# Performance work log

Measured on AMD Instinct MI355X. Metric: run time of the kernel, lower is better.

The kernel has to match this reference:

```python
import jax, jax.numpy as jnp
import numpy as np

B, T, NX, NZ, D = 8, 16, 256, 64, 1024
HEADS, DHEAD = 8, 64
INNER = HEADS * DHEAD
EPS = 1e-5


def layer_norm(x, g, b):
    mu = jnp.mean(x, axis=-1, keepdims=True)
    var = jnp.var(x, axis=-1, keepdims=True)
    return (x - mu) * jax.lax.rsqrt(var + EPS) * g + b


def setup_inputs() -> dict:
    key = jax.random.key(0)
    ks = jax.random.split(key, 8)
    x = jax.random.normal(ks[0], (B, T, NX, D), dtype=jnp.float32)
    latents = jax.random.normal(ks[1], (B, T, NZ, D), dtype=jnp.float32)
    mask = jax.random.randint(ks[2], (B, T), 0, 2).astype(bool)
    # learned params (torch Linear weight (out,in) stored transposed as (in,out))
    s = 1.0 / np.sqrt(D)
    Wq = jax.random.uniform(ks[3], (D, INNER), jnp.float32, -s, s)
    Wkv = jax.random.uniform(ks[4], (D, 2 * INNER), jnp.float32, -s, s)
    si = 1.0 / np.sqrt(INNER)
    Wo = jax.random.uniform(ks[5], (INNER, D), jnp.float32, -si, si)
    gm = jnp.ones((D,), jnp.float32); bm = jnp.zeros((D,), jnp.float32)
    gl = jnp.ones((D,), jnp.float32); bl = jnp.zeros((D,), jnp.float32)
    return {"x": x, "latents": latents, "mask": mask,
            "gm": gm, "bm": bm, "gl": gl, "bl": bl,
            "Wq": Wq, "Wkv": Wkv, "Wo": Wo}


def _forward(x, latents, mask, gm, bm, gl, bl, Wq, Wkv, Wo):
    scale = DHEAD ** (-0.5)
    xn = layer_norm(x, gm, bm)            # (b,T,Nx,D)
    zn = layer_norm(latents, gl, bl)      # (b,T,Nz,D)
    q = zn @ Wq                           # (b,T,Nz,inner)
    kv = jnp.concatenate([xn, zn], axis=-2) @ Wkv   # (b,T,Nx+Nz,2*inner)
    k, v = jnp.split(kv, 2, axis=-1)

    def to_heads(t):  # b t n (h d) -> b h t n d
        b_, t_, n_, _ = t.shape
        return t.reshape(b_, t_, n_, HEADS, DHEAD).transpose(0, 3, 1, 2, 4)

    q, k, v = to_heads(q), to_heads(k), to_heads(v)
    mb = mask[:, None, :, None, None]     # (b,1,T,1,1) bool
    q = q * scale * mb
    sim = jnp.einsum('bhtid,bhtjd->bhtij', q, k)   # (b,h,T,Nz,Nx+Nz)
    # key_keep is mask broadcast over all keys; row_has_key == mask for the row's t
    sim = jnp.where(mb, sim, -jnp.inf)
    sim = jnp.where(mb, sim, 0.0)          # zero-fallback for fully-masked rows
    sim = sim - jax.lax.stop_gradient(jnp.max(sim, axis=-1, keepdims=True))
    attn = jax.nn.softmax(sim, axis=-1)
    attn = attn * mb
    out = jnp.einsum('bhtij,bhtjd->bhtid', attn, v)  # (b,h,T,Nz,d)
    out = out.transpose(0, 2, 3, 1, 4).reshape(out.shape[0], out.shape[2], out.shape[3], INNER)
    out = out * mask[:, :, None, None]
    return out @ Wo                        # (b,T,Nz,D)


def reference(x, latents, mask, gm, bm, gl, bl, Wq, Wkv, Wo):
    return _forward(x, latents, mask, gm, bm, gl, bl, Wq, Wkv, Wo)
```

## Files before the change

### kernel.cpp

```cpp
#include <hip/hip_runtime.h>
#include <stdint.h>
#include <stddef.h>

#define B_      8
#define T_      16
#define NX_     256
#define NZ_     64
#define D_      1024
#define HEADS_  8
#define DHEAD_  64
#define INNER_  512
#define NKEY_   320
#define NBT_    128

typedef __attribute__((ext_vector_type(8))) short     short8;
typedef __attribute__((ext_vector_type(4))) float     f32x4;
typedef __attribute__((ext_vector_type(8))) unsigned short u16x8;

__device__ __forceinline__ unsigned short f2bf(float f) {
    union { float f; unsigned int u; } v; v.f = f;
    unsigned int u = v.u;
    return (unsigned short)((u + 0x7fffu + ((u >> 16) & 1u)) >> 16);
}

__device__ __forceinline__ void async16(unsigned short* lds, const unsigned short* g) {
    __builtin_amdgcn_global_load_lds(
        (const __attribute__((address_space(1))) void*)g,
        (__attribute__((address_space(3))) void*)lds, 16, 0, 0);
}

__device__ __forceinline__ int xcd_swz(int bid, int L) {
    int q = L >> 3, r = L & 7;
    int xcd = bid & 7, idx = bid >> 3;
    return (xcd < r ? xcd * (q + 1) : r * (q + 1) + (xcd - r) * q) + idx;
}

__global__ __launch_bounds__(256) void prep_kernel(
        const float* __restrict__ Wq, const float* __restrict__ Wkv,
        const float* __restrict__ Wo, const unsigned char* __restrict__ mraw,
        unsigned short* __restrict__ WqT, unsigned short* __restrict__ WkvT,
        unsigned short* __restrict__ WoT,
        int* __restrict__ maskN, int* __restrict__ meta,
        int* __restrict__ liveBt, int* __restrict__ grpSrc,
        int* __restrict__ grpOut) {
    if (blockIdx.x == 8192) {
        int l = threadIdx.x;
        if (l >= 64) return;
        unsigned char b0 = mraw[l];
        unsigned char b1 = mraw[l + 64];
        bool nz = ((l & 3) != 0 && b0 != 0) || (((l + 64) & 3) != 0 && b1 != 0);
        unsigned long long ball = __ballot(nz ? 1 : 0);
        bool isBool = (ball != 0ull);
        int v0, v1;
        if (isBool) { v0 = b0; v1 = b1; }
        else        { v0 = mraw[4 * l]; v1 = mraw[4 * (l + 64)]; }
        v0 = v0 ? 1 : 0; v1 = v1 ? 1 : 0;
        maskN[l]      = v0;
        maskN[l + 64] = v1;
        unsigned long long B0 = __ballot(v0), B1 = __ballot(v1);
        int n0 = __popcll(B0);
        int nl = n0 + __popcll(B1);
        unsigned long long below = (1ull << l) - 1ull;
        if (v0) {
            int p = __popcll(B0 & below);
            liveBt[p] = l;
            #pragma unroll
            for (int g = 0; g < 5; g++) {
                grpSrc[5 * p + g] = l * NKEY_ + g * 64;
                grpOut[5 * p + g] = (l << 16) | (g * 64);
            }
        }
        if (v1) {
            int p = n0 + __popcll(B1 & below);
            int bt = l + 64;
            liveBt[p] = bt;
            #pragma unroll
            for (int g = 0; g < 5; g++) {
                grpSrc[5 * p + g] = bt * NKEY_ + g * 64;
                grpOut[5 * p + g] = (bt << 16) | (g * 64);
            }
        }
        if (l == 0) {
            int lastBt = 0;
            if (B1) lastBt = 64 + (63 - __clzll(B1));
            else if (B0) lastBt = 63 - __clzll(B0);
            int ng = 5 * nl;
            if (nl & 1) liveBt[nl] = lastBt;
            if (ng & 1) { grpSrc[ng] = lastBt * NKEY_ + 256;
                          grpOut[ng] = (lastBt << 16) | 256; }
            meta[0] = nl;
            meta[1] = (ng + 1) >> 1;
            meta[2] = (nl + 1) >> 1;
        }
        return;
    }
    size_t id = (size_t)blockIdx.x * 256 + threadIdx.x;
    if (id < 524288) {
        int n = (int)(id >> 10), k = (int)(id & 1023);
        WqT[id] = f2bf(Wq[(size_t)k * 512 + n]);
    } else if (id < 524288 + 1048576) {
        size_t j = id - 524288;
        int n = (int)(j >> 10), k = (int)(j & 1023);
        WkvT[j] = f2bf(Wkv[(size_t)k * 1024 + n]);
    } else {
        size_t j = id - 1572864;
        int n = (int)(j >> 9), k = (int)(j & 511);
        WoT[j] = f2bf(Wo[(size_t)k * 1024 + n]);
    }
}

__global__ __launch_bounds__(256) void ln_kernel(
        const float* __restrict__ x, const float* __restrict__ lat,
        const float* __restrict__ gm, const float* __restrict__ bm,
        const float* __restrict__ gl, const float* __restrict__ bl,
        const int* __restrict__ maskN,
        unsigned short* __restrict__ kvin) {
    int row = blockIdx.x;
    const float* src; unsigned short* dst; const float* g; const float* b;
    int bt;
    if (row < NBT_ * NX_) {
        bt = row >> 8;
        src = x + (size_t)row * D_;
        dst = kvin + ((size_t)bt * NKEY_ + (row & 255)) * D_;
        g = gm; b = bm;
    } else {
        int r = row - NBT_ * NX_;
        bt = r >> 6;
        src = lat + (size_t)r * D_;
        dst = kvin + ((size_t)bt * NKEY_ + 256 + (r & 63)) * D_;
        g = gl; b = bl;
    }
    if (!maskN[bt]) return;
    int t = threadIdx.x;
    float4 v = reinterpret_cast<const float4*>(src)[t];
    float s  = v.x + v.y + v.z + v.w;
    float sq = v.x * v.x + v.y * v.y + v.z * v.z + v.w * v.w;
    #pragma unroll
    for (int off = 32; off > 0; off >>= 1) {
        s  += __shfl_down(s, off);
        sq += __shfl_down(sq, off);
    }
    __shared__ float red[8];
    int wid = t >> 6;
    if ((t & 63) == 0) { red[wid] = s; red[4 + wid] = sq; }
    __syncthreads();
    float stot = red[0] + red[1] + red[2] + red[3];
    float qtot = red[4] + red[5] + red[6] + red[7];
    float mean = stot * (1.0f / 1024.0f);
    float var  = qtot * (1.0f / 1024.0f) - mean * mean;
    float rstd = rsqrtf(var + 1e-5f);
    float4 gv = reinterpret_cast<const float4*>(g)[t];
    float4 bv = reinterpret_cast<const float4*>(b)[t];
    ushort4 o;
    o.x = f2bf((v.x - mean) * rstd * gv.x + bv.x);
    o.y = f2bf((v.y - mean) * rstd * gv.y + bv.y);
    o.z = f2bf((v.z - mean) * rstd * gv.z + bv.z);
    o.w = f2bf((v.w - mean) * rstd * gv.w + bv.w);
    *reinterpret_cast<ushort4*>(dst + 4 * t) = o;
}

template<int MODE>
__global__ __launch_bounds__(256, 4) void gemm128_kernel(
        const unsigned short* __restrict__ A,
        const unsigned short* __restrict__ BT,
        const int* __restrict__ meta,
        const int* __restrict__ liveBt,
        const int* __restrict__ grpSrc,
        const int* __restrict__ grpOut,
        unsigned short* __restrict__ o_q,
        unsigned short* __restrict__ o_k,
        unsigned short* __restrict__ o_v,
        float* __restrict__ o_f) {
    constexpr int K     = (MODE == 2) ? 512 : 1024;
    constexpr int NSTEP = K / 32;
    constexpr int NTSH  = (MODE == 0) ? 2 : 3;

    int lim = (MODE == 1) ? meta[1] : meta[2];
    int L = lim << NTSH;
    int bid = blockIdx.x;
    if (bid >= L) return;
    int wg = xcd_swz(bid, L);
    int mt = wg >> NTSH;
    int nt = wg & ((1 << NTSH) - 1);
    int n0 = nt * 128;
    int t = threadIdx.x;
    int lane = t & 63, wid = t >> 6;
    int lr = lane & 15, lg = lane >> 4;
    int wm = wid >> 1, wn = wid & 1;

    __shared__ __align__(16) unsigned short As[2][4096];
    __shared__ __align__(16) unsigned short Bs[2][4096];

    const unsigned short* aptr[2];
    const unsigned short* bptr[2];
    int grp = wid >> 1;
    #pragma unroll
    for (int j = 0; j < 2; j++) {
        int R   = (wid * 2 + j) * 16 + (lane >> 2);
        int rin = R & 63;
        size_t srow;
        if (MODE == 0) {
            int bt = liveBt[2 * mt + grp];
            srow = (size_t)bt * NKEY_ + 256 + rin;
        } else if (MODE == 1) {
            srow = (size_t)grpSrc[2 * mt + grp] + rin;
        } else {
            int bt = liveBt[2 * mt + grp];
            srow = (size_t)bt * 64 + rin;
        }
        aptr[j] = A  + srow * K + (lane & 3) * 8;
        bptr[j] = BT + (size_t)(n0 + R) * K + (lane & 3) * 8;
    }

    f32x4 acc[4][4];
    #pragma unroll
    for (int i = 0; i < 4; i++)
        #pragma unroll
        for (int j = 0; j < 4; j++) acc[i][j] = (f32x4){0.f, 0.f, 0.f, 0.f};

    auto stage = [&](int buf) {
        #pragma unroll
        for (int j = 0; j < 2; j++) {
            async16(&As[buf][(wid * 2 + j) * 512], aptr[j]);
            async16(&Bs[buf][(wid * 2 + j) * 512], bptr[j]);
            aptr[j] += 32; bptr[j] += 32;
        }
    };
    auto compute = [&](int buf) {
        short8 af[4], bf[4];
        #pragma unroll
        for (int mi = 0; mi < 4; mi++)
            af[mi] = *reinterpret_cast<const short8*>(
                &As[buf][(wm * 64 + mi * 16 + lr) * 32 + lg * 8]);
        #pragma unroll
        for (int ni = 0; ni < 4; ni++)
            bf[ni] = *reinterpret_cast<const short8*>(
                &Bs[buf][(wn * 64 + ni * 16 + lr) * 32 + lg * 8]);
        #pragma unroll
        for (int mi = 0; mi < 4; mi++)
            #pragma unroll
            for (int ni = 0; ni < 4; ni++)
                acc[mi][ni] = __builtin_amdgcn_mfma_f32_16x16x32_bf16(
                    af[mi], bf[ni], acc[mi][ni], 0, 0, 0);
    };

    #define FULL_STEP(CUR)                                              \
        stage((CUR) ^ 1);                                               \
        asm volatile("s_waitcnt vmcnt(4)" ::: "memory");                \
        __builtin_amdgcn_s_barrier();                                   \
        compute(CUR);                                                   \
        asm volatile("s_waitcnt lgkmcnt(0)" ::: "memory");              \
        __builtin_amdgcn_s_barrier();

    stage(0);
    #pragma unroll 1
    for (int ks2 = 0; ks2 < NSTEP / 2 - 1; ks2++) {
        FULL_STEP(0)
        FULL_STEP(1)
    }
    FULL_STEP(0)
    asm volatile("s_waitcnt vmcnt(0)" ::: "memory");
    __builtin_amdgcn_s_barrier();
    compute(1);
    #undef FULL_STEP

    #pragma unroll
    for (int mi = 0; mi < 4; mi++)
        #pragma unroll
        for (int ni = 0; ni < 4; ni++) {
            int rr = mi * 16 + lg * 4;
            int c  = n0 + wn * 64 + ni * 16 + lr;
            if (MODE == 0) {
                int bt = liveBt[2 * mt + wm];
                #pragma unroll
                for (int r = 0; r < 4; r++)
                    o_q[((size_t)bt * 64 + rr + r) * 512 + c] =
                        f2bf(acc[mi][ni][r] * 0.125f);
            } else if (MODE == 1) {
                int enc = grpOut[2 * mt + wm];
                int bt = enc >> 16, krow = (enc & 0xffff) + rr;
                if (c < 512) {
                    #pragma unroll
                    for (int r = 0; r < 4; r++)
                        o_k[((size_t)bt * NKEY_ + krow + r) * 512 + c] =
                            f2bf(acc[mi][ni][r]);
                } else {
                    ushort4 pv;
                    pv.x = f2bf(acc[mi][ni][0]); pv.y = f2bf(acc[mi][ni][1]);
                    pv.z = f2bf(acc[mi][ni][2]); pv.w = f2bf(acc[mi][ni][3]);
                    *reinterpret_cast<ushort4*>(
                        o_v + ((size_t)bt * 512 + (c - 512)) * NKEY_ + krow) = pv;
                }
            } else {
                int bt = liveBt[2 * mt + wm];
                #pragma unroll
                for (int r = 0; r < 4; r++)
                    o_f[((size_t)bt * 64 + rr + r) * 1024 + c] = acc[mi][ni][r];
            }
        }
}

__global__ __launch_bounds__(256) void attn_kernel(
        const unsigned short* __restrict__ q,
        const unsigned short* __restrict__ kbuf,
        const unsigned short* __restrict__ vbuf,
        const int* __restrict__ meta,
        const int* __restrict__ liveBt,
        const int* __restrict__ maskN,
        unsigned short* __restrict__ ao,
        float* __restrict__ out_f) {
    int bid = blockIdx.x;
    if (bid >= 1024) {
        int bt = bid - 1024;
        if (maskN[bt]) return;
        float4* p = reinterpret_cast<float4*>(out_f + (size_t)bt * 65536);
        float4 z = make_float4(0.f, 0.f, 0.f, 0.f);
        #pragma unroll
        for (int k = 0; k < 64; k++) p[k * 256 + threadIdx.x] = z;
        return;
    }
    int L = meta[0] << 3;
    if (bid >= L) return;
    int wg = xcd_swz(bid, L);
    int i = wg >> 3, h = wg & 7;
    int bt = liveBt[i];
    int t = threadIdx.x, w = t >> 6, lane = t & 63;
    int lr = lane & 15, lg = lane >> 4;
    __shared__ __align__(16) unsigned short attn_s[4][16][328];

    const unsigned short* qrow = q + ((size_t)bt * 64 + w * 16 + lr) * 512 + h * 64;
    short8 qa0 = *reinterpret_cast<const short8*>(qrow + lg * 8);
    short8 qa1 = *reinterpret_cast<const short8*>(qrow + 32 + lg * 8);

    f32x4 acc[20];
    #pragma unroll
    for (int i2 = 0; i2 < 20; i2++) acc[i2] = (f32x4){0.f, 0.f, 0.f, 0.f};

    const unsigned short* kb = kbuf + (size_t)bt * NKEY_ * 512 + h * 64;
    #pragma unroll
    for (int nt2 = 0; nt2 < 20; nt2++) {
        const unsigned short* krow = kb + (size_t)(nt2 * 16 + lr) * 512;
        short8 b0 = *reinterpret_cast<const short8*>(krow + lg * 8);
        short8 b1 = *reinterpret_cast<const short8*>(krow + 32 + lg * 8);
        acc[nt2] = __builtin_amdgcn_mfma_f32_16x16x32_bf16(qa0, b0, acc[nt2], 0, 0, 0);
        acc[nt2] = __builtin_amdgcn_mfma_f32_16x16x32_bf16(qa1, b1, acc[nt2], 0, 0, 0);
    }

    float mx[4], sm[4];
    #pragma unroll
    for (int r = 0; r < 4; r++) mx[r] = -1e30f;
    #pragma unroll
    for (int nt2 = 0; nt2 < 20; nt2++)
        #pragma unroll
        for (int r = 0; r < 4; r++) mx[r] = fmaxf(mx[r], acc[nt2][r]);
    #pragma unroll
    for (int r = 0; r < 4; r++) {
        #pragma unroll
        for (int off = 1; off < 16; off <<= 1)
            mx[r] = fmaxf(mx[r], __shfl_xor(mx[r], off));
        sm[r] = 0.f;
    }
    #pragma unroll
    for (int nt2 = 0; nt2 < 20; nt2++)
        #pragma unroll
        for (int r = 0; r < 4; r++) {
            float p = __expf(acc[nt2][r] - mx[r]);
            acc[nt2][r] = p;
            sm[r] += p;
        }
    #pragma unroll
    for (int r = 0; r < 4; r++) {
        #pragma unroll
        for (int off = 1; off < 16; off <<= 1)
            sm[r] += __shfl_xor(sm[r], off);
        sm[r] = 1.0f / sm[r];
    }
    #pragma unroll
    for (int nt2 = 0; nt2 < 20; nt2++)
        #pragma unroll
        for (int r = 0; r < 4; r++)
            attn_s[w][lg * 4 + r][nt2 * 16 + lr] = f2bf(acc[nt2][r] * sm[r]);
    __syncthreads();

    f32x4 o[4];
    #pragma unroll
    for (int i2 = 0; i2 < 4; i2++) o[i2] = (f32x4){0.f, 0.f, 0.f, 0.f};
    const unsigned short* vb = vbuf + (size_t)bt * 512 * NKEY_ + (size_t)h * 64 * NKEY_;
    #pragma unroll
    for (int kc = 0; kc < 10; kc++) {
        short8 pa = *reinterpret_cast<const short8*>(&attn_s[w][lr][kc * 32 + lg * 8]);
        #pragma unroll
        for (int ni = 0; ni < 4; ni++) {
            short8 vf = *reinterpret_cast<const short8*>(
                vb + (size_t)(ni * 16 + lr) * NKEY_ + kc * 32 + lg * 8);
            o[ni] = __builtin_amdgcn_mfma_f32_16x16x32_bf16(pa, vf, o[ni], 0, 0, 0);
        }
    }
    #pragma unroll
    for (int ni = 0; ni < 4; ni++)
        #pragma unroll
        for (int r = 0; r < 4; r++)
            ao[((size_t)bt * 64 + w * 16 + lg * 4 + r) * 512 + h * 64 + ni * 16 + lr] =
                f2bf(o[ni][r]);
}

extern "C" void kernel_launch(void* const* d_in, const int* in_sizes, int n_in,
                              void* d_out, int out_size, void* d_ws, size_t ws_size,
                              hipStream_t stream) {
    const float* x            = (const float*)d_in[0];
    const float* lat          = (const float*)d_in[1];
    const unsigned char* mraw = (const unsigned char*)d_in[2];
    const float* gm           = (const float*)d_in[3];
    const float* bm           = (const float*)d_in[4];
    const float* gl           = (const float*)d_in[5];
    const float* bl           = (const float*)d_in[6];
    const float* Wq           = (const float*)d_in[7];
    const float* Wkv          = (const float*)d_in[8];
    const float* Wo           = (const float*)d_in[9];
    float* out = (float*)d_out;

    char* ws = (char*)d_ws;
    int* maskN  = (int*)(ws + 0);
    int* meta   = (int*)(ws + 512);
    int* liveBt = (int*)(ws + 1024);
    int* grpSrc = (int*)(ws + 2048);
    int* grpOut = (int*)(ws + 5120);
    size_t off = 8192;
    unsigned short* WqT  = (unsigned short*)(ws + off); off += 1048576;
    unsigned short* WkvT = (unsigned short*)(ws + off); off += 2097152;
    unsigned short* WoT  = (unsigned short*)(ws + off); off += 1048576;
    unsigned short* kvin = (unsigned short*)(ws + off); off += 83886080;
    unsigned short* qb   = (unsigned short*)(ws + off); off += 8388608;
    unsigned short* kb   = (unsigned short*)(ws + off); off += 41943040;
    unsigned short* vb   = (unsigned short*)(ws + off); off += 41943040;
    unsigned short* ab   = (unsigned short*)(ws + off); off += 8388608;

    hipLaunchKernelGGL(prep_kernel, dim3(8193),  dim3(256), 0, stream,
                       Wq, Wkv, Wo, mraw, WqT, WkvT, WoT,
                       maskN, meta, liveBt, grpSrc, grpOut);
    hipLaunchKernelGGL(ln_kernel,   dim3(40960), dim3(256), 0, stream,
                       x, lat, gm, bm, gl, bl, maskN, kvin);
    hipLaunchKernelGGL((gemm128_kernel<0>), dim3(256),  dim3(256), 0, stream,
                       kvin, WqT,  meta, liveBt, grpSrc, grpOut, qb, kb, vb, out);
    hipLaunchKernelGGL((gemm128_kernel<1>), dim3(2560), dim3(256), 0, stream,
                       kvin, WkvT, meta, liveBt, grpSrc, grpOut, qb, kb, vb, out);
    hipLaunchKernelGGL(attn_kernel,         dim3(1152), dim3(256), 0, stream,
                       qb, kb, vb, meta, liveBt, maskN, ab, out);
    hipLaunchKernelGGL((gemm128_kernel<2>), dim3(512),  dim3(256), 0, stream,
                       ab, WoT,  meta, liveBt, grpSrc, grpOut, qb, kb, vb, out);
}
```

Baseline: 151.2 us.

## Merge weight prep with layernorm and fuse Q and KV projection GEMMs

Folds the weight transpose/convert work and the layernorm into one launch. LN blocks now recompute each row's live flag straight from the raw mask instead of waiting on maskN from the earlier kernel. Also runs the Q-projection and KV-projection GEMMs as one grid dispatched by block index. This removes two kernel launches and the tail gaps between them, at the cost of redundant mask decoding in every LN block plus an extra __syncthreads.

```diff
diff --git a/kernel.cpp b/kernel.cpp
--- a/kernel.cpp
+++ b/kernel.cpp
@@ -15,7 +15,6 @@
 
 typedef __attribute__((ext_vector_type(8))) short     short8;
 typedef __attribute__((ext_vector_type(4))) float     f32x4;
-typedef __attribute__((ext_vector_type(8))) unsigned short u16x8;
 
 __device__ __forceinline__ unsigned short f2bf(float f) {
     union { float f; unsigned int u; } v; v.f = f;
@@ -35,15 +34,35 @@
     return (xcd < r ? xcd * (q + 1) : r * (q + 1) + (xcd - r) * q) + idx;
 }
 
-__global__ __launch_bounds__(256) void prep_kernel(
+__global__ __launch_bounds__(256) void prep_ln_kernel(
         const float* __restrict__ Wq, const float* __restrict__ Wkv,
         const float* __restrict__ Wo, const unsigned char* __restrict__ mraw,
+        const float* __restrict__ x, const float* __restrict__ lat,
+        const float* __restrict__ gm, const float* __restrict__ bm,
+        const float* __restrict__ gl, const float* __restrict__ bl,
         unsigned short* __restrict__ WqT, unsigned short* __restrict__ WkvT,
-        unsigned short* __restrict__ WoT,
+        unsigned short* __restrict__ WoT, unsigned short* __restrict__ kvin,
         int* __restrict__ maskN, int* __restrict__ meta,
         int* __restrict__ liveBt, int* __restrict__ grpSrc,
         int* __restrict__ grpOut) {
-    if (blockIdx.x == 8192) {
+    int bid = blockIdx.x;
+    if (bid < 8192) {
+        size_t id = (size_t)bid * 256 + threadIdx.x;
+        if (id < 524288) {
+            int n = (int)(id >> 10), k = (int)(id & 1023);
+            WqT[id] = f2bf(Wq[(size_t)k * 512 + n]);
+        } else if (id < 524288 + 1048576) {
+            size_t j = id - 524288;
+            int n = (int)(j >> 10), k = (int)(j & 1023);
+            WkvT[j] = f2bf(Wkv[(size_t)k * 1024 + n]);
+        } else {
+            size_t j = id - 1572864;
+            int n = (int)(j >> 9), k = (int)(j & 511);
+            WoT[j] = f2bf(Wo[(size_t)k * 1024 + n]);
+        }
+        return;
+    }
+    if (bid == 8192) {
         int l = threadIdx.x;
         if (l >= 64) return;
         unsigned char b0 = mraw[l];
@@ -94,28 +113,7 @@
         }
         return;
     }
-    size_t id = (size_t)blockIdx.x * 256 + threadIdx.x;
-    if (id < 524288) {
-        int n = (int)(id >> 10), k = (int)(id & 1023);
-        WqT[id] = f2bf(Wq[(size_t)k * 512 + n]);
-    } else if (id < 524288 + 1048576) {
-        size_t j = id - 524288;
-        int n = (int)(j >> 10), k = (int)(j & 1023);
-        WkvT[j] = f2bf(Wkv[(size_t)k * 1024 + n]);
-    } else {
-        size_t j = id - 1572864;
-        int n = (int)(j >> 9), k = (int)(j & 511);
-        WoT[j] = f2bf(Wo[(size_t)k * 1024 + n]);
-    }
-}
-
-__global__ __launch_bounds__(256) void ln_kernel(
-        const float* __restrict__ x, const float* __restrict__ lat,
-        const float* __restrict__ gm, const float* __restrict__ bm,
-        const float* __restrict__ gl, const float* __restrict__ bl,
-        const int* __restrict__ maskN,
-        unsigned short* __restrict__ kvin) {
-    int row = blockIdx.x;
+    int row = bid - 8193;
     const float* src; unsigned short* dst; const float* g; const float* b;
     int bt;
     if (row < NBT_ * NX_) {
@@ -130,8 +128,21 @@
         dst = kvin + ((size_t)bt * NKEY_ + 256 + (r & 63)) * D_;
         g = gl; b = bl;
     }
-    if (!maskN[bt]) return;
     int t = threadIdx.x;
+    __shared__ int liveFlag;
+    if (t < 64) {
+        unsigned char c0 = mraw[t];
+        unsigned char c1 = mraw[t + 64];
+        bool nz = ((t & 3) != 0 && c0 != 0) || (((t + 64) & 3) != 0 && c1 != 0);
+        unsigned long long ball = __ballot(nz ? 1 : 0);
+        bool isBool = (ball != 0ull);
+        if (t == 0) {
+            int v = isBool ? mraw[bt] : mraw[4 * bt];
+            liveFlag = v ? 1 : 0;
+        }
+    }
+    __syncthreads();
+    if (!liveFlag) return;
     float4 v = reinterpret_cast<const float4*>(src)[t];
     float s  = v.x + v.y + v.z + v.w;
     float sq = v.x * v.x + v.y * v.y + v.z * v.z + v.w * v.w;
@@ -160,7 +171,8 @@
 }
 
 template<int MODE>
-__global__ __launch_bounds__(256, 4) void gemm128_kernel(
+__device__ __forceinline__ void gemm128_body(
+        int bid, unsigned short* As, unsigned short* Bs,
         const unsigned short* __restrict__ A,
         const unsigned short* __restrict__ BT,
         const int* __restrict__ meta,
@@ -177,7 +189,6 @@
 
     int lim = (MODE == 1) ? meta[1] : meta[2];
     int L = lim << NTSH;
-    int bid = blockIdx.x;
     if (bid >= L) return;
     int wg = xcd_swz(bid, L);
     int mt = wg >> NTSH;
@@ -187,9 +198,6 @@
     int lane = t & 63, wid = t >> 6;
     int lr = lane & 15, lg = lane >> 4;
     int wm = wid >> 1, wn = wid & 1;
-
-    __shared__ __align__(16) unsigned short As[2][4096];
-    __shared__ __align__(16) unsigned short Bs[2][4096];
 
     const unsigned short* aptr[2];
     const unsigned short* bptr[2];
@@ -221,8 +229,8 @@
     auto stage = [&](int buf) {
         #pragma unroll
         for (int j = 0; j < 2; j++) {
-            async16(&As[buf][(wid * 2 + j) * 512], aptr[j]);
-            async16(&Bs[buf][(wid * 2 + j) * 512], bptr[j]);
+            async16(As + buf * 4096 + (wid * 2 + j) * 512, aptr[j]);
+            async16(Bs + buf * 4096 + (wid * 2 + j) * 512, bptr[j]);
             aptr[j] += 32; bptr[j] += 32;
         }
     };
@@ -231,11 +239,11 @@
         #pragma unroll
         for (int mi = 0; mi < 4; mi++)
             af[mi] = *reinterpret_cast<const short8*>(
-                &As[buf][(wm * 64 + mi * 16 + lr) * 32 + lg * 8]);
+                &As[buf * 4096 + (wm * 64 + mi * 16 + lr) * 32 + lg * 8]);
         #pragma unroll
         for (int ni = 0; ni < 4; ni++)
             bf[ni] = *reinterpret_cast<const short8*>(
-                &Bs[buf][(wn * 64 + ni * 16 + lr) * 32 + lg * 8]);
+                &Bs[buf * 4096 + (wn * 64 + ni * 16 + lr) * 32 + lg * 8]);
         #pragma unroll
         for (int mi = 0; mi < 4; mi++)
             #pragma unroll
@@ -300,6 +308,43 @@
         }
 }
 
+__global__ __launch_bounds__(256, 4) void gemm_kvq_kernel(
+        const unsigned short* __restrict__ kvin,
+        const unsigned short* __restrict__ WkvT,
+        const unsigned short* __restrict__ WqT,
+        const int* __restrict__ meta,
+        const int* __restrict__ liveBt,
+        const int* __restrict__ grpSrc,
+        const int* __restrict__ grpOut,
+        unsigned short* __restrict__ o_q,
+        unsigned short* __restrict__ o_k,
+        unsigned short* __restrict__ o_v) {
+    __shared__ __align__(16) unsigned short As[2 * 4096];
+    __shared__ __align__(16) unsigned short Bs[2 * 4096];
+    int bid = blockIdx.x;
+    if (bid < 2560)
+        gemm128_body<1>(bid, As, Bs, kvin, WkvT, meta, liveBt, grpSrc, grpOut,
+                        o_q, o_k, o_v, (float*)0);
+    else
+        gemm128_body<0>(bid - 2560, As, Bs, kvin, WqT, meta, liveBt, grpSrc,
+                        grpOut, o_q, o_k, o_v, (float*)0);
+}
+
+__global__ __launch_bounds__(256, 4) void gemm_out_kernel(
+        const unsigned short* __restrict__ ab,
+        const unsigned short* __restrict__ WoT,
+        const int* __restrict__ meta,
+        const int* __restrict__ liveBt,
+        const int* __restrict__ grpSrc,
+        const int* __restrict__ grpOut,
+        float* __restrict__ o_f) {
+    __shared__ __align__(16) unsigned short As[2 * 4096];
+    __shared__ __align__(16) unsigned short Bs[2 * 4096];
+    gemm128_body<2>(blockIdx.x, As, Bs, ab, WoT, meta, liveBt, grpSrc, grpOut,
+                    (unsigned short*)0, (unsigned short*)0, (unsigned short*)0,
+                    o_f);
+}
+
 __global__ __launch_bounds__(256) void attn_kernel(
         const unsigned short* __restrict__ q,
         const unsigned short* __restrict__ kbuf,
@@ -435,17 +480,14 @@
     unsigned short* vb   = (unsigned short*)(ws + off); off += 41943040;
     unsigned short* ab   = (unsigned short*)(ws + off); off += 8388608;
 
-    hipLaunchKernelGGL(prep_kernel, dim3(8193),  dim3(256), 0, stream,
-                       Wq, Wkv, Wo, mraw, WqT, WkvT, WoT,
-                       maskN, meta, liveBt, grpSrc, grpOut);
-    hipLaunchKernelGGL(ln_kernel,   dim3(40960), dim3(256), 0, stream,
-                       x, lat, gm, bm, gl, bl, maskN, kvin);
-    hipLaunchKernelGGL((gemm128_kernel<0>), dim3(256),  dim3(256), 0, stream,
-                       kvin, WqT,  meta, liveBt, grpSrc, grpOut, qb, kb, vb, out);
-    hipLaunchKernelGGL((gemm128_kernel<1>), dim3(2560), dim3(256), 0, stream,
-                       kvin, WkvT, meta, liveBt, grpSrc, grpOut, qb, kb, vb, out);
-    hipLaunchKernelGGL(attn_kernel,         dim3(1152), dim3(256), 0, stream,
+    hipLaunchKernelGGL(prep_ln_kernel, dim3(49153), dim3(256), 0, stream,
+                       Wq, Wkv, Wo, mraw, x, lat, gm, bm, gl, bl,
+                       WqT, WkvT, WoT, kvin, maskN, meta, liveBt, grpSrc, grpOut);
+    hipLaunchKernelGGL(gemm_kvq_kernel, dim3(2816), dim3(256), 0, stream,
+                       kvin, WkvT, WqT, meta, liveBt, grpSrc, grpOut,
+                       qb, kb, vb);
+    hipLaunchKernelGGL(attn_kernel,     dim3(1152), dim3(256), 0, stream,
                        qb, kb, vb, meta, liveBt, maskN, ab, out);
-    hipLaunchKernelGGL((gemm128_kernel<2>), dim3(512),  dim3(256), 0, stream,
-                       ab, WoT,  meta, liveBt, grpSrc, grpOut, qb, kb, vb, out);
-}
+    hipLaunchKernelGGL(gemm_out_kernel, dim3(512),  dim3(256), 0, stream,
+                       ab, WoT, meta, liveBt, grpSrc, grpOut, out);
+}
```

Result: faster. 142.0 us (-6.1%).
